# Optimization experiments

Measured on AMD Instinct MI355X. Metric: run time of the kernel, lower is better.

Reference implementation:

```python
import jax, jax.numpy as jnp
import numpy as np

B, A, N, K, F, E = 2, 5, 1000, 16, 256, 3


def setup_inputs() -> dict:
    key = jax.random.key(0)
    ks = jax.random.split(key, 6)
    nfeature = jax.random.normal(ks[0], (B, A, N, F), dtype=jnp.float32)
    nn_idx = jax.random.randint(ks[1], (B, A, N, K), 0, N)
    etype = jax.random.randint(ks[2], (B, A, N, K), 0, E)
    W = jax.random.normal(ks[3], (A, E, F, F), dtype=jnp.float32) * (1.0 / np.sqrt(F))
    b = jnp.zeros((A, E, F), dtype=jnp.float32)
    W1 = jax.random.normal(ks[4], (A, F, F), dtype=jnp.float32) * (1.0 / np.sqrt(F))
    W2 = jax.random.normal(ks[5], (A, F, F), dtype=jnp.float32) * (1.0 / np.sqrt(F))
    b2 = jnp.zeros((A, F), dtype=jnp.float32)
    return {"nfeature": nfeature, "nn_idx": nn_idx, "etype": etype,
            "W": W, "b": b, "W1": W1, "W2": W2, "b2": b2}


def reference(nfeature, nn_idx, etype, W, b, W1, W2, b2):
    Bs, As, Ns, Fs = nfeature.shape
    Ks = nn_idx.shape[-1]
    Es = W.shape[1]
    # gather neighbor features per anchor: [B, A, N, K, F]
    idx = nn_idx.reshape(Bs, As, Ns * Ks, 1)
    nbr = jnp.take_along_axis(nfeature, idx, axis=2).reshape(Bs, As, Ns, Ks, Fs)
    onehot = jax.nn.one_hot(etype, Es, dtype=nfeature.dtype)  # [B, A, N, K, E]
    # edge-type-specific pointwise transform (loop over small fixed E)
    msg = jnp.zeros((Bs, As, Ns, Ks, Fs), dtype=nfeature.dtype)
    for e in range(Es):
        y = jnp.einsum('bankf,afg->bankg', nbr, W[:, e]) + b[:, e][None, :, None, None, :]
        msg = msg + onehot[..., e:e + 1] * y
    pw = jax.nn.relu(msg.mean(axis=3))  # aggregate over K neighbors -> [B, A, N, F]
    # hop: mix each anchor with the summed 'mutual' feature
    mutual = pw.sum(axis=1)  # [B, N, F]
    hop = jax.nn.relu(jnp.einsum('banf,afg->bang', pw, W1)
                      + jnp.einsum('bnf,afg->bang', mutual, W2)
                      + b2[None, :, None, :])
    return hop + nfeature  # residual add
```

## Files before the change

kernel.cpp:

```cpp
#include <hip/hip_runtime.h>

typedef float f32x4 __attribute__((ext_vector_type(4)));
typedef __bf16 bf16x8 __attribute__((ext_vector_type(8)));
typedef unsigned short u16x4 __attribute__((ext_vector_type(4)));
typedef unsigned short u16x8 __attribute__((ext_vector_type(8)));

constexpr int B_ = 2, A_ = 5, N_ = 1000, K_ = 16, F_ = 256, E_ = 3;
constexpr int TILE = 16;
constexpr int RTOT = B_ * N_;
constexpr int NT   = RTOT / TILE;
constexpr int KS1  = (E_ * F_) / 32;
constexpr int KS2  = (2 * F_) / 32;
constexpr int NTL  = F_ / 16;

constexpr int GATHER_BLOCKS = (A_ * RTOT) / 4;
constexpr int PACK_THREADS  = A_ * KS1 * NTL * 64 + A_ * KS2 * NTL * 64;
constexpr int PACK_BLOCKS   = PACK_THREADS / 256;

constexpr size_t SZ_WPK  = (size_t)A_ * KS1 * NTL * 512 * 2;
constexpr size_t OFF_W12 = SZ_WPK;
constexpr size_t SZ_W12  = (size_t)A_ * KS2 * NTL * 512 * 2;
constexpr size_t OFF_PWB = OFF_W12 + SZ_W12;
constexpr size_t SZ_PWB  = (size_t)A_ * RTOT * F_ * 2;
constexpr size_t OFF_SG  = OFF_PWB + SZ_PWB;
constexpr size_t SZ_SG   = (size_t)A_ * RTOT * (E_ * F_) * 2;
constexpr size_t OFF_CNT = OFF_SG + SZ_SG;

__device__ __forceinline__ unsigned short f2bf(float x) {
  unsigned int u = __builtin_bit_cast(unsigned int, x);
  u += 0x7fffu + ((u >> 16) & 1u);
  return (unsigned short)(u >> 16);
}
__device__ __forceinline__ float bf2f(unsigned short h) {
  return __builtin_bit_cast(float, (unsigned int)h << 16);
}

__global__ __launch_bounds__(256) void k_gather_pack(
    const float* __restrict__ nf, const int* __restrict__ nn_idx,
    const int* __restrict__ et, const float* __restrict__ W,
    const float* __restrict__ W1, const float* __restrict__ W2,
    unsigned short* __restrict__ Sg, float* __restrict__ CNTS,
    unsigned short* __restrict__ wpk, unsigned short* __restrict__ w12)
{
  if (blockIdx.x < GATHER_BLOCKS) {
    const int task = blockIdx.x * 4 + (threadIdx.x >> 6);
    const int lane = threadIdx.x & 63;
    const int a  = task / RTOT;
    const int rg = task - a * RTOT;
    const int bb = rg / N_;
    const int n  = rg - bb * N_;
    const int eoff = ((bb * A_ + a) * N_ + n) * K_;

    int4 iv[4], ev[4];
#pragma unroll
    for (int q = 0; q < 4; ++q) {
      iv[q] = *reinterpret_cast<const int4*>(nn_idx + eoff + q * 4);
      ev[q] = *reinterpret_cast<const int4*>(et + eoff + q * 4);
    }
    const float* __restrict__ slab =
        nf + (size_t)(bb * A_ + a) * N_ * F_ + lane * 4;
    f32x4 a0 = {0.f, 0.f, 0.f, 0.f}, a1 = a0, a2 = a0;
    int c0 = 0, c1 = 0, c2 = 0;
#pragma unroll
    for (int q = 0; q < 4; ++q) {
#pragma unroll
      for (int j = 0; j < 4; ++j) {
        const int id = ((const int*)&iv[q])[j];
        const int e  = ((const int*)&ev[q])[j];
        const f32x4 v = *reinterpret_cast<const f32x4*>(slab + (size_t)id * F_);
        if (e == 0)      { a0 += v; ++c0; }
        else if (e == 1) { a1 += v; ++c1; }
        else             { a2 += v; ++c2; }
      }
    }
    unsigned short* __restrict__ row = Sg + ((size_t)a * RTOT + rg) * 768;
    const int sw = (rg & 7) << 3;
    u16x4 p0, p1, p2;
#pragma unroll
    for (int j = 0; j < 4; ++j) {
      p0[j] = f2bf(a0[j]); p1[j] = f2bf(a1[j]); p2[j] = f2bf(a2[j]);
    }
    *reinterpret_cast<u16x4*>(row + ((0 * F_ + lane * 4) ^ sw)) = p0;
    *reinterpret_cast<u16x4*>(row + ((1 * F_ + lane * 4) ^ sw)) = p1;
    *reinterpret_cast<u16x4*>(row + ((2 * F_ + lane * 4) ^ sw)) = p2;
    if (lane == 0) {
      f32x4 c = {(float)c0, (float)c1, (float)c2, 0.f};
      *reinterpret_cast<f32x4*>(CNTS + (size_t)task * 4) = c;
    }
  } else {
    const int id = (blockIdx.x - GATHER_BLOCKS) * 256 + threadIdx.x;
    const int T1 = A_ * KS1 * NTL * 64;
    const int T2 = A_ * KS2 * NTL * 64;
    if (id < T1) {
      const int lane = id & 63, nt = (id >> 6) & 15;
      const int r = id >> 10, t = r % KS1, a = r / KS1;
      const int k0 = t * 32 + (lane >> 4) * 8;
      const int n  = nt * 16 + (lane & 15);
      const float* src = W + ((size_t)a * E_ * F_ + k0) * F_ + n;
      u16x8 v;
#pragma unroll
      for (int j = 0; j < 8; ++j) v[j] = f2bf(src[(size_t)j * F_]);
      *reinterpret_cast<u16x8*>(wpk + (size_t)id * 8) = v;
    } else if (id < T1 + T2) {
      const int p = id - T1;
      const int lane = p & 63, nt = (p >> 6) & 15;
      const int r = p >> 10, t = r % KS2, a = r / KS2;
      const int k0 = t * 32 + (lane >> 4) * 8;
      const int n  = nt * 16 + (lane & 15);
      u16x8 v;
#pragma unroll
      for (int j = 0; j < 8; ++j) {
        const int k = k0 + j;
        const float s = (k < F_) ? W1[((size_t)a * F_ + k) * F_ + n]
                                 : W2[((size_t)a * F_ + (k - F_)) * F_ + n];
        v[j] = f2bf(s);
      }
      *reinterpret_cast<u16x8*>(w12 + (size_t)p * 8) = v;
    }
  }
}

__global__ __launch_bounds__(256) void k_gemm1(
    const unsigned short* __restrict__ Sg, const float* __restrict__ CNTS,
    const unsigned short* __restrict__ wpk, const float* __restrict__ bias,
    unsigned short* __restrict__ pwb)
{
  __shared__ alignas(16) unsigned short S[TILE * E_ * F_];
  __shared__ float CNT[TILE][4];
  const int a   = blockIdx.y;
  const int r0  = blockIdx.x * TILE;
  const int tid = threadIdx.x;

  const unsigned short* src = Sg + ((size_t)a * RTOT + r0) * 768;
#pragma unroll
  for (int it = 0; it < 6; ++it) {
    const int off = (it * 256 + tid) * 8;
    __builtin_amdgcn_global_load_lds(
        (const __attribute__((address_space(1))) unsigned int*)(src + off),
        (__attribute__((address_space(3))) unsigned int*)(S + off), 16, 0, 0);
  }
  if (tid < TILE)
    *reinterpret_cast<f32x4*>(&CNT[tid][0]) =
        *reinterpret_cast<const f32x4*>(CNTS + (size_t)(a * RTOT + r0 + tid) * 4);
  __syncthreads();

  const int lane = tid & 63, wv = tid >> 6;
  const int arow = lane & 15, kg = lane >> 4;
  const unsigned short* __restrict__ Wp = wpk + (size_t)a * KS1 * NTL * 512;
  f32x4 acc[4];
#pragma unroll
  for (int m = 0; m < 4; ++m) acc[m] = (f32x4){0.f, 0.f, 0.f, 0.f};
  const int ssw = (arow & 7) << 3;
#pragma unroll
  for (int t = 0; t < KS1; ++t) {
    const int si = (arow * 768 + t * 32 + kg * 8) ^ ssw;
    const bf16x8 af = *reinterpret_cast<const bf16x8*>(&S[si]);
#pragma unroll
    for (int m = 0; m < 4; ++m) {
      const int nt = wv * 4 + m;
      const bf16x8 bfr = *reinterpret_cast<const bf16x8*>(
          Wp + ((size_t)(t * NTL + nt) * 64 + lane) * 8);
      acc[m] = __builtin_amdgcn_mfma_f32_16x16x32_bf16(af, bfr, acc[m], 0, 0, 0);
    }
  }

  const float* __restrict__ ba = bias + a * E_ * F_;
#pragma unroll
  for (int m = 0; m < 4; ++m) {
    const int col = (wv * 4 + m) * 16 + arow;
    const float b0 = ba[col], b1 = ba[F_ + col], b2v = ba[2 * F_ + col];
#pragma unroll
    for (int rr = 0; rr < 4; ++rr) {
      const int row = kg * 4 + rr;
      const int r   = r0 + row;
      float x = (acc[m][rr] + CNT[row][0] * b0 + CNT[row][1] * b1 +
                 CNT[row][2] * b2v) * (1.0f / K_);
      x = fmaxf(x, 0.f);
      pwb[((size_t)a * RTOT + r) * F_ + (col ^ ((row & 7) << 3))] = f2bf(x);
    }
  }
}

__global__ __launch_bounds__(256) void k_hop_mfma(
    const unsigned short* __restrict__ pwb, const unsigned short* __restrict__ w12,
    const float* __restrict__ b2, const float* __restrict__ nf,
    float* __restrict__ out)
{
  __shared__ alignas(16) unsigned short S2[2 * TILE * F_];
  const int a   = blockIdx.y;
  const int r0  = blockIdx.x * TILE;
  const int tid = threadIdx.x;

  const unsigned short* srcP = pwb + ((size_t)a * RTOT + r0) * F_;
#pragma unroll
  for (int it = 0; it < 2; ++it) {
    const int off = (it * 256 + tid) * 8;
    __builtin_amdgcn_global_load_lds(
        (const __attribute__((address_space(1))) unsigned int*)(srcP + off),
        (__attribute__((address_space(3))) unsigned int*)(S2 + off), 16, 0, 0);
  }
#pragma unroll
  for (int it = 0; it < 2; ++it) {
    const int i = (it * 256 + tid) * 8;
    float s[8] = {0.f, 0.f, 0.f, 0.f, 0.f, 0.f, 0.f, 0.f};
#pragma unroll
    for (int a2 = 0; a2 < A_; ++a2) {
      const u16x8 v = *reinterpret_cast<const u16x8*>(
          pwb + ((size_t)a2 * RTOT + r0) * F_ + i);
#pragma unroll
      for (int j = 0; j < 8; ++j) s[j] += bf2f(v[j]);
    }
    u16x8 o;
#pragma unroll
    for (int j = 0; j < 8; ++j) o[j] = f2bf(s[j]);
    *reinterpret_cast<u16x8*>(&S2[TILE * F_ + i]) = o;
  }
  __syncthreads();

  const int lane = tid & 63, wv = tid >> 6;
  const int arow = lane & 15, kg = lane >> 4;
  const unsigned short* __restrict__ Wp = w12 + (size_t)a * KS2 * NTL * 512;
  f32x4 acc[4];
#pragma unroll
  for (int m = 0; m < 4; ++m) acc[m] = (f32x4){0.f, 0.f, 0.f, 0.f};
  const int ssw = (arow & 7) << 3;
#pragma unroll
  for (int t = 0; t < KS2; ++t) {
    const int half = t >> 3;
    const int kk   = (t & 7) * 32;
    const int si   = half * (TILE * F_) + arow * F_ + ((kk + kg * 8) ^ ssw);
    const bf16x8 af = *reinterpret_cast<const bf16x8*>(&S2[si]);
#pragma unroll
    for (int m = 0; m < 4; ++m) {
      const int nt = wv * 4 + m;
      const bf16x8 bfr = *reinterpret_cast<const bf16x8*>(
          Wp + ((size_t)(t * NTL + nt) * 64 + lane) * 8);
      acc[m] = __builtin_amdgcn_mfma_f32_16x16x32_bf16(af, bfr, acc[m], 0, 0, 0);
    }
  }

#pragma unroll
  for (int m = 0; m < 4; ++m) {
    const int col = (wv * 4 + m) * 16 + arow;
    const float bb2 = b2[a * F_ + col];
#pragma unroll
    for (int rr = 0; rr < 4; ++rr) {
      const int row = kg * 4 + rr;
      const int r = r0 + row, bb = r / N_, n = r - bb * N_;
      const size_t o = ((size_t)(bb * A_ + a) * N_ + n) * F_ + col;
      out[o] = fmaxf(acc[m][rr] + bb2, 0.f) + nf[o];
    }
  }
}

extern "C" void kernel_launch(void* const* d_in, const int* in_sizes, int n_in,
                              void* d_out, int out_size, void* d_ws, size_t ws_size,
                              hipStream_t stream)
{
  const float* nf     = (const float*)d_in[0];
  const int*   nn_idx = (const int*)  d_in[1];
  const int*   et     = (const int*)  d_in[2];
  const float* W      = (const float*)d_in[3];
  const float* bias   = (const float*)d_in[4];
  const float* W1     = (const float*)d_in[5];
  const float* W2     = (const float*)d_in[6];
  const float* b2     = (const float*)d_in[7];
  float* out = (float*)d_out;

  unsigned short* wpk  = (unsigned short*)d_ws;
  unsigned short* w12  = (unsigned short*)((char*)d_ws + OFF_W12);
  unsigned short* pwb  = (unsigned short*)((char*)d_ws + OFF_PWB);
  unsigned short* Sg   = (unsigned short*)((char*)d_ws + OFF_SG);
  float*          CNTS = (float*)((char*)d_ws + OFF_CNT);

  k_gather_pack<<<dim3(GATHER_BLOCKS + PACK_BLOCKS), 256, 0, stream>>>(
      nf, nn_idx, et, W, W1, W2, Sg, CNTS, wpk, w12);

  dim3 gtile(NT, A_);
  k_gemm1<<<gtile, 256, 0, stream>>>(Sg, CNTS, wpk, bias, pwb);
  k_hop_mfma<<<gtile, 256, 0, stream>>>(pwb, w12, b2, nf, out);
}
```

Measured before the change: 53.25 us.

## Use 32-row tiles with 512 threads, pad rows, and swizzle blocks across XCDs

The row tile in both GEMM kernels grows from 16 to 32, with 8 waves each computing a 2x2 block of MFMA outputs, so each weight fragment loaded from global memory feeds two MFMAs. This halves weight traffic per row. Rows are padded to 2016 so the tile divides evenly. Blocks are linearised and remapped (swz315, plus a remap in gather) so that neighbouring work lands on the same XCD for L2 locality. The cost is fewer blocks (315), more LDS per block, and padding rows that are gathered redundantly and masked out on store.

```diff
diff --git a/kernel.cpp b/kernel.cpp
--- a/kernel.cpp
+++ b/kernel.cpp
@@ -6,14 +6,16 @@
 typedef unsigned short u16x8 __attribute__((ext_vector_type(8)));
 
 constexpr int B_ = 2, A_ = 5, N_ = 1000, K_ = 16, F_ = 256, E_ = 3;
-constexpr int TILE = 16;
 constexpr int RTOT = B_ * N_;
-constexpr int NT   = RTOT / TILE;
+constexpr int ROWS = 2016;
+constexpr int TIL  = 32;
+constexpr int NT   = ROWS / TIL;
+constexpr int GBL  = NT * A_;
 constexpr int KS1  = (E_ * F_) / 32;
 constexpr int KS2  = (2 * F_) / 32;
 constexpr int NTL  = F_ / 16;
 
-constexpr int GATHER_BLOCKS = (A_ * RTOT) / 4;
+constexpr int GATHER_BLOCKS = (A_ * ROWS) / 4;
 constexpr int PACK_THREADS  = A_ * KS1 * NTL * 64 + A_ * KS2 * NTL * 64;
 constexpr int PACK_BLOCKS   = PACK_THREADS / 256;
 
@@ -21,9 +23,9 @@
 constexpr size_t OFF_W12 = SZ_WPK;
 constexpr size_t SZ_W12  = (size_t)A_ * KS2 * NTL * 512 * 2;
 constexpr size_t OFF_PWB = OFF_W12 + SZ_W12;
-constexpr size_t SZ_PWB  = (size_t)A_ * RTOT * F_ * 2;
+constexpr size_t SZ_PWB  = (size_t)A_ * ROWS * F_ * 2;
 constexpr size_t OFF_SG  = OFF_PWB + SZ_PWB;
-constexpr size_t SZ_SG   = (size_t)A_ * RTOT * (E_ * F_) * 2;
+constexpr size_t SZ_SG   = (size_t)A_ * ROWS * (E_ * F_) * 2;
 constexpr size_t OFF_CNT = OFF_SG + SZ_SG;
 
 __device__ __forceinline__ unsigned short f2bf(float x) {
@@ -33,6 +35,10 @@
 }
 __device__ __forceinline__ float bf2f(unsigned short h) {
   return __builtin_bit_cast(float, (unsigned int)h << 16);
+}
+__device__ __forceinline__ int swz315(int bid) {
+  const int xcd = bid & 7, idx = bid >> 3;
+  return (xcd < 3 ? xcd * 40 : 120 + (xcd - 3) * 39) + idx;
 }
 
 __global__ __launch_bounds__(256) void k_gather_pack(
@@ -43,10 +49,13 @@
     unsigned short* __restrict__ wpk, unsigned short* __restrict__ w12)
 {
   if (blockIdx.x < GATHER_BLOCKS) {
-    const int task = blockIdx.x * 4 + (threadIdx.x >> 6);
+    const int bid  = blockIdx.x;
+    const int nbid = (bid & 7) * (GATHER_BLOCKS / 8) + (bid >> 3);
+    const int task = nbid * 4 + (threadIdx.x >> 6);
     const int lane = threadIdx.x & 63;
-    const int a  = task / RTOT;
-    const int rg = task - a * RTOT;
+    const int a  = task / ROWS;
+    const int rp = task - a * ROWS;
+    const int rg = rp < RTOT ? rp : RTOT - 1;
     const int bb = rg / N_;
     const int n  = rg - bb * N_;
     const int eoff = ((bb * A_ + a) * N_ + n) * K_;
@@ -73,8 +82,8 @@
         else             { a2 += v; ++c2; }
       }
     }
-    unsigned short* __restrict__ row = Sg + ((size_t)a * RTOT + rg) * 768;
-    const int sw = (rg & 7) << 3;
+    unsigned short* __restrict__ row = Sg + ((size_t)a * ROWS + rp) * 768;
+    const int sw = (rp & 7) << 3;
     u16x4 p0, p1, p2;
 #pragma unroll
     for (int j = 0; j < 4; ++j) {
@@ -120,135 +129,162 @@
   }
 }
 
-__global__ __launch_bounds__(256) void k_gemm1(
+__global__ __launch_bounds__(512) void k_gemm1(
     const unsigned short* __restrict__ Sg, const float* __restrict__ CNTS,
     const unsigned short* __restrict__ wpk, const float* __restrict__ bias,
     unsigned short* __restrict__ pwb)
 {
-  __shared__ alignas(16) unsigned short S[TILE * E_ * F_];
-  __shared__ float CNT[TILE][4];
-  const int a   = blockIdx.y;
-  const int r0  = blockIdx.x * TILE;
+  __shared__ alignas(16) unsigned short S[TIL * E_ * F_];
+  __shared__ float CNT[TIL][4];
+  const int lin = swz315(blockIdx.x);
+  const int a   = lin / NT;
+  const int r0  = (lin - a * NT) * TIL;
   const int tid = threadIdx.x;
 
-  const unsigned short* src = Sg + ((size_t)a * RTOT + r0) * 768;
+  const unsigned short* src = Sg + ((size_t)a * ROWS + r0) * 768;
 #pragma unroll
   for (int it = 0; it < 6; ++it) {
-    const int off = (it * 256 + tid) * 8;
+    const int off = (it * 512 + tid) * 8;
     __builtin_amdgcn_global_load_lds(
         (const __attribute__((address_space(1))) unsigned int*)(src + off),
         (__attribute__((address_space(3))) unsigned int*)(S + off), 16, 0, 0);
   }
-  if (tid < TILE)
+  if (tid < TIL)
     *reinterpret_cast<f32x4*>(&CNT[tid][0]) =
-        *reinterpret_cast<const f32x4*>(CNTS + (size_t)(a * RTOT + r0 + tid) * 4);
+        *reinterpret_cast<const f32x4*>(CNTS + (size_t)(a * ROWS + r0 + tid) * 4);
   __syncthreads();
 
   const int lane = tid & 63, wv = tid >> 6;
   const int arow = lane & 15, kg = lane >> 4;
   const unsigned short* __restrict__ Wp = wpk + (size_t)a * KS1 * NTL * 512;
-  f32x4 acc[4];
-#pragma unroll
-  for (int m = 0; m < 4; ++m) acc[m] = (f32x4){0.f, 0.f, 0.f, 0.f};
+  f32x4 acc[2][2];
+#pragma unroll
+  for (int c = 0; c < 2; ++c)
+#pragma unroll
+    for (int mb = 0; mb < 2; ++mb) acc[c][mb] = (f32x4){0.f, 0.f, 0.f, 0.f};
   const int ssw = (arow & 7) << 3;
 #pragma unroll
   for (int t = 0; t < KS1; ++t) {
-    const int si = (arow * 768 + t * 32 + kg * 8) ^ ssw;
-    const bf16x8 af = *reinterpret_cast<const bf16x8*>(&S[si]);
-#pragma unroll
-    for (int m = 0; m < 4; ++m) {
-      const int nt = wv * 4 + m;
+    bf16x8 af[2];
+#pragma unroll
+    for (int mb = 0; mb < 2; ++mb) {
+      const int si = ((mb * 16 + arow) * 768 + t * 32 + kg * 8) ^ ssw;
+      af[mb] = *reinterpret_cast<const bf16x8*>(&S[si]);
+    }
+#pragma unroll
+    for (int c = 0; c < 2; ++c) {
+      const int nt = wv * 2 + c;
       const bf16x8 bfr = *reinterpret_cast<const bf16x8*>(
           Wp + ((size_t)(t * NTL + nt) * 64 + lane) * 8);
-      acc[m] = __builtin_amdgcn_mfma_f32_16x16x32_bf16(af, bfr, acc[m], 0, 0, 0);
+#pragma unroll
+      for (int mb = 0; mb < 2; ++mb)
+        acc[c][mb] = __builtin_amdgcn_mfma_f32_16x16x32_bf16(af[mb], bfr, acc[c][mb], 0, 0, 0);
     }
   }
 
   const float* __restrict__ ba = bias + a * E_ * F_;
 #pragma unroll
-  for (int m = 0; m < 4; ++m) {
-    const int col = (wv * 4 + m) * 16 + arow;
+  for (int c = 0; c < 2; ++c) {
+    const int col = (wv * 2 + c) * 16 + arow;
     const float b0 = ba[col], b1 = ba[F_ + col], b2v = ba[2 * F_ + col];
 #pragma unroll
-    for (int rr = 0; rr < 4; ++rr) {
-      const int row = kg * 4 + rr;
-      const int r   = r0 + row;
-      float x = (acc[m][rr] + CNT[row][0] * b0 + CNT[row][1] * b1 +
-                 CNT[row][2] * b2v) * (1.0f / K_);
-      x = fmaxf(x, 0.f);
-      pwb[((size_t)a * RTOT + r) * F_ + (col ^ ((row & 7) << 3))] = f2bf(x);
-    }
-  }
-}
-
-__global__ __launch_bounds__(256) void k_hop_mfma(
+    for (int mb = 0; mb < 2; ++mb) {
+#pragma unroll
+      for (int rr = 0; rr < 4; ++rr) {
+        const int row = mb * 16 + kg * 4 + rr;
+        const int r   = r0 + row;
+        float x = (acc[c][mb][rr] + CNT[row][0] * b0 + CNT[row][1] * b1 +
+                   CNT[row][2] * b2v) * (1.0f / K_);
+        x = fmaxf(x, 0.f);
+        pwb[((size_t)a * ROWS + r) * F_ + (col ^ ((row & 7) << 3))] = f2bf(x);
+      }
+    }
+  }
+}
+
+__global__ __launch_bounds__(512) void k_hop_mfma(
     const unsigned short* __restrict__ pwb, const unsigned short* __restrict__ w12,
     const float* __restrict__ b2, const float* __restrict__ nf,
     float* __restrict__ out)
 {
-  __shared__ alignas(16) unsigned short S2[2 * TILE * F_];
-  const int a   = blockIdx.y;
-  const int r0  = blockIdx.x * TILE;
+  __shared__ alignas(16) unsigned short S2[2 * TIL * F_];
+  const int lin = swz315(blockIdx.x);
+  const int a   = lin / NT;
+  const int r0  = (lin - a * NT) * TIL;
   const int tid = threadIdx.x;
 
-  const unsigned short* srcP = pwb + ((size_t)a * RTOT + r0) * F_;
+  const unsigned short* srcP = pwb + ((size_t)a * ROWS + r0) * F_;
 #pragma unroll
   for (int it = 0; it < 2; ++it) {
-    const int off = (it * 256 + tid) * 8;
+    const int off = (it * 512 + tid) * 8;
     __builtin_amdgcn_global_load_lds(
         (const __attribute__((address_space(1))) unsigned int*)(srcP + off),
         (__attribute__((address_space(3))) unsigned int*)(S2 + off), 16, 0, 0);
   }
 #pragma unroll
   for (int it = 0; it < 2; ++it) {
-    const int i = (it * 256 + tid) * 8;
+    const int i = (it * 512 + tid) * 8;
     float s[8] = {0.f, 0.f, 0.f, 0.f, 0.f, 0.f, 0.f, 0.f};
 #pragma unroll
     for (int a2 = 0; a2 < A_; ++a2) {
       const u16x8 v = *reinterpret_cast<const u16x8*>(
-          pwb + ((size_t)a2 * RTOT + r0) * F_ + i);
+          pwb + ((size_t)a2 * ROWS + r0) * F_ + i);
 #pragma unroll
       for (int j = 0; j < 8; ++j) s[j] += bf2f(v[j]);
     }
     u16x8 o;
 #pragma unroll
     for (int j = 0; j < 8; ++j) o[j] = f2bf(s[j]);
-    *reinterpret_cast<u16x8*>(&S2[TILE * F_ + i]) = o;
+    *reinterpret_cast<u16x8*>(&S2[TIL * F_ + i]) = o;
   }
   __syncthreads();
 
   const int lane = tid & 63, wv = tid >> 6;
   const int arow = lane & 15, kg = lane >> 4;
   const unsigned short* __restrict__ Wp = w12 + (size_t)a * KS2 * NTL * 512;
-  f32x4 acc[4];
-#pragma unroll
-  for (int m = 0; m < 4; ++m) acc[m] = (f32x4){0.f, 0.f, 0.f, 0.f};
+  f32x4 acc[2][2];
+#pragma unroll
+  for (int c = 0; c < 2; ++c)
+#pragma unroll
+    for (int mb = 0; mb < 2; ++mb) acc[c][mb] = (f32x4){0.f, 0.f, 0.f, 0.f};
   const int ssw = (arow & 7) << 3;
 #pragma unroll
   for (int t = 0; t < KS2; ++t) {
     const int half = t >> 3;
     const int kk   = (t & 7) * 32;
-    const int si   = half * (TILE * F_) + arow * F_ + ((kk + kg * 8) ^ ssw);
-    const bf16x8 af = *reinterpret_cast<const bf16x8*>(&S2[si]);
-#pragma unroll
-    for (int m = 0; m < 4; ++m) {
-      const int nt = wv * 4 + m;
+    bf16x8 af[2];
+#pragma unroll
+    for (int mb = 0; mb < 2; ++mb) {
+      const int si = half * (TIL * F_) + (mb * 16 + arow) * F_ + ((kk + kg * 8) ^ ssw);
+      af[mb] = *reinterpret_cast<const bf16x8*>(&S2[si]);
+    }
+#pragma unroll
+    for (int c = 0; c < 2; ++c) {
+      const int nt = wv * 2 + c;
       const bf16x8 bfr = *reinterpret_cast<const bf16x8*>(
           Wp + ((size_t)(t * NTL + nt) * 64 + lane) * 8);
-      acc[m] = __builtin_amdgcn_mfma_f32_16x16x32_bf16(af, bfr, acc[m], 0, 0, 0);
-    }
-  }
-
-#pragma unroll
-  for (int m = 0; m < 4; ++m) {
-    const int col = (wv * 4 + m) * 16 + arow;
+#pragma unroll
+      for (int mb = 0; mb < 2; ++mb)
+        acc[c][mb] = __builtin_amdgcn_mfma_f32_16x16x32_bf16(af[mb], bfr, acc[c][mb], 0, 0, 0);
+    }
+  }
+
+#pragma unroll
+  for (int c = 0; c < 2; ++c) {
+    const int col = (wv * 2 + c) * 16 + arow;
     const float bb2 = b2[a * F_ + col];
 #pragma unroll
-    for (int rr = 0; rr < 4; ++rr) {
-      const int row = kg * 4 + rr;
-      const int r = r0 + row, bb = r / N_, n = r - bb * N_;
-      const size_t o = ((size_t)(bb * A_ + a) * N_ + n) * F_ + col;
-      out[o] = fmaxf(acc[m][rr] + bb2, 0.f) + nf[o];
+    for (int mb = 0; mb < 2; ++mb) {
+#pragma unroll
+      for (int rr = 0; rr < 4; ++rr) {
+        const int row = mb * 16 + kg * 4 + rr;
+        const int r   = r0 + row;
+        if (r < RTOT) {
+          const int bb = r / N_, n = r - bb * N_;
+          const size_t o = ((size_t)(bb * A_ + a) * N_ + n) * F_ + col;
+          out[o] = fmaxf(acc[c][mb][rr] + bb2, 0.f) + nf[o];
+        }
+      }
     }
   }
 }
@@ -276,7 +312,6 @@
   k_gather_pack<<<dim3(GATHER_BLOCKS + PACK_BLOCKS), 256, 0, stream>>>(
       nf, nn_idx, et, W, W1, W2, Sg, CNTS, wpk, w12);
 
-  dim3 gtile(NT, A_);
-  k_gemm1<<<gtile, 256, 0, stream>>>(Sg, CNTS, wpk, bias, pwb);
-  k_hop_mfma<<<gtile, 256, 0, stream>>>(pwb, w12, b2, nf, out);
-}
+  k_gemm1<<<dim3(GBL), 512, 0, stream>>>(Sg, CNTS, wpk, bias, pwb);
+  k_hop_mfma<<<dim3(GBL), 512, 0, stream>>>(pwb, w12, b2, nf, out);
+}
```

Result: faster. 47.97 us (-9.9%).
